# Kernel optimization log

Hardware: AMD Instinct MI355X
Metric: run time of the kernel (lower is better)

The kernel has to match this reference:

```python
import jax, jax.numpy as jnp
import numpy as np
from jax import lax

N_EMBD = 4096
N_EXPERTS = 64


def setup_inputs() -> dict:
    key = jax.random.key(0)
    kx, kw = jax.random.split(key)
    x = jax.random.normal(kx, (4, 4096, N_EMBD), dtype=jnp.float32)
    # nn.Linear(n_embd, n_experts, bias=False) -> weight shape [n_experts, n_embd]
    W = jax.random.normal(kw, (N_EXPERTS, N_EMBD), dtype=jnp.float32) * (1.0 / np.sqrt(N_EMBD))
    return {"x": x, "W": W}


def reference(x, W):
    # logits = x @ W^T : [B, S, n_experts]
    logits = jnp.einsum('bsd,ed->bse', x, W)
    topk_vals, topk_idx = lax.top_k(logits, 2)  # [B, S, 2]
    gates = jax.nn.softmax(topk_vals, axis=-1)  # softmax over just the top-2 values
    return (topk_idx, gates)
```

## Files before the change

kernel.cpp:

```cpp
#include <hip/hip_runtime.h>
#include <math.h>

#define N_EMBD    4096
#define N_EXPERTS 64
#define N_TOKENS  16384
#define TAU       1e-3f

typedef __attribute__((ext_vector_type(8))) short bf16x8;
typedef __attribute__((ext_vector_type(4))) float f32x4;

#define MFMA16 __builtin_amdgcn_mfma_f32_16x16x32_bf16

__device__ __forceinline__ void split_pair(float f0, float f1,
                                           unsigned& hpack, unsigned& lpack) {
    unsigned u0 = __builtin_bit_cast(unsigned, f0);
    unsigned u1 = __builtin_bit_cast(unsigned, f1);
    unsigned r0 = u0 + 0x7FFFu + ((u0 >> 16) & 1u);
    unsigned r1 = u1 + 0x7FFFu + ((u1 >> 16) & 1u);
    hpack = (r0 >> 16) | (r1 & 0xFFFF0000u);
    float h0 = __builtin_bit_cast(float, r0 & 0xFFFF0000u);
    float h1 = __builtin_bit_cast(float, r1 & 0xFFFF0000u);
    float l0 = f0 - h0;
    float l1 = f1 - h1;
    unsigned v0 = __builtin_bit_cast(unsigned, l0);
    unsigned v1 = __builtin_bit_cast(unsigned, l1);
    unsigned s0 = v0 + 0x7FFFu + ((v0 >> 16) & 1u);
    unsigned s1 = v1 + 0x7FFFu + ((v1 >> 16) & 1u);
    lpack = (s0 >> 16) | (s1 & 0xFFFF0000u);
}

__global__ void wt_pack(const float* __restrict__ W, float4* __restrict__ Wt4) {
    int tid = blockIdx.x * blockDim.x + threadIdx.x;
    int e  = tid >> 10;
    int k4 = tid & 1023;
    Wt4[k4 * 64 + e] = ((const float4*)W)[e * 1024 + k4];
}

__global__ void w_pack_bf16(const float* __restrict__ W,
                            uint4* __restrict__ Bpack,
                            int* __restrict__ flags) {
    int tid = blockIdx.x * blockDim.x + threadIdx.x;
    if (tid == 0) flags[0] = 0;
    int lane = tid & 63;
    int nt   = (tid >> 6) & 3;
    int ks   = tid >> 8;
    int e = nt * 16 + (lane & 15);
    int k = ks * 32 + ((lane >> 4) << 3);
    const float* src = W + (size_t)e * N_EMBD + k;
    uint4 hp, lp;
    split_pair(src[0], src[1], hp.x, lp.x);
    split_pair(src[2], src[3], hp.y, lp.y);
    split_pair(src[4], src[5], hp.z, lp.z);
    split_pair(src[6], src[7], hp.w, lp.w);
    size_t F = (size_t)ks * 8 + nt * 2;
    Bpack[F * 64 + lane]       = hp;
    Bpack[(F + 1) * 64 + lane] = lp;
}

__device__ __forceinline__ void compute_step(
        float4 A0, float4 A1,
        uint4 B0, uint4 B1, uint4 B2, uint4 B3,
        uint4 B4, uint4 B5, uint4 B6, uint4 B7,
        f32x4& c0, f32x4& c1, f32x4& c2, f32x4& c3) {
    uint4 hu, lu;
    split_pair(A0.x, A0.y, hu.x, lu.x);
    split_pair(A0.z, A0.w, hu.y, lu.y);
    split_pair(A1.x, A1.y, hu.z, lu.z);
    split_pair(A1.z, A1.w, hu.w, lu.w);
    bf16x8 ah = __builtin_bit_cast(bf16x8, hu);
    bf16x8 al = __builtin_bit_cast(bf16x8, lu);
    bf16x8 bh, bl;
    bh = __builtin_bit_cast(bf16x8, B0); bl = __builtin_bit_cast(bf16x8, B1);
    c0 = MFMA16(ah, bh, c0, 0, 0, 0);
    c0 = MFMA16(ah, bl, c0, 0, 0, 0);
    c0 = MFMA16(al, bh, c0, 0, 0, 0);
    bh = __builtin_bit_cast(bf16x8, B2); bl = __builtin_bit_cast(bf16x8, B3);
    c1 = MFMA16(ah, bh, c1, 0, 0, 0);
    c1 = MFMA16(ah, bl, c1, 0, 0, 0);
    c1 = MFMA16(al, bh, c1, 0, 0, 0);
    bh = __builtin_bit_cast(bf16x8, B4); bl = __builtin_bit_cast(bf16x8, B5);
    c2 = MFMA16(ah, bh, c2, 0, 0, 0);
    c2 = MFMA16(ah, bl, c2, 0, 0, 0);
    c2 = MFMA16(al, bh, c2, 0, 0, 0);
    bh = __builtin_bit_cast(bf16x8, B6); bl = __builtin_bit_cast(bf16x8, B7);
    c3 = MFMA16(ah, bh, c3, 0, 0, 0);
    c3 = MFMA16(ah, bl, c3, 0, 0, 0);
    c3 = MFMA16(al, bh, c3, 0, 0, 0);
}

__global__ __launch_bounds__(256, 2) void router_mfma(
        const float* __restrict__ x,
        const uint4* __restrict__ Bpack,
        float* __restrict__ partial) {
    const int lane = threadIdx.x & 63;
    const int wv   = threadIdx.x >> 6;
    const int kh   = blockIdx.x & 1;
    const int tg   = (blockIdx.x >> 1) * 4 + wv;
    const int tok0 = tg * 16;

    const float4* pa = (const float4*)(x + (size_t)(tok0 + (lane & 15)) * N_EMBD
                                         + kh * 2048 + ((lane >> 4) << 3));
    const uint4* pb = Bpack + (size_t)(kh * 64 * 8) * 64 + lane;

    f32x4 acc0 = {0.f,0.f,0.f,0.f}, acc1 = {0.f,0.f,0.f,0.f};
    f32x4 acc2 = {0.f,0.f,0.f,0.f}, acc3 = {0.f,0.f,0.f,0.f};

    uint4 ba0, ba1, ba2, ba3, ba4, ba5, ba6, ba7;
    uint4 bb0, bb1, bb2, bb3, bb4, bb5, bb6, bb7;
    float4 a0a, a1a, a0b, a1b;

#define LOADB(P, s) { const uint4* _q = pb + (size_t)(s) * 512;               \
    P##0 = _q[0];   P##1 = _q[64];  P##2 = _q[128]; P##3 = _q[192];           \
    P##4 = _q[256]; P##5 = _q[320]; P##6 = _q[384]; P##7 = _q[448]; }
#define LOADA(A0, A1, s) { A0 = pa[(s) * 8]; A1 = pa[(s) * 8 + 1]; }

    LOADB(ba, 0); LOADA(a0a, a1a, 0);
    for (int s = 0; s < 64; s += 2) {
        LOADB(bb, s + 1); LOADA(a0b, a1b, s + 1);
        compute_step(a0a, a1a, ba0, ba1, ba2, ba3, ba4, ba5, ba6, ba7,
                     acc0, acc1, acc2, acc3);
        __syncthreads();
        if (s < 62) { LOADB(ba, s + 2); LOADA(a0a, a1a, s + 2); }
        compute_step(a0b, a1b, bb0, bb1, bb2, bb3, bb4, bb5, bb6, bb7,
                     acc0, acc1, acc2, acc3);
        __syncthreads();
    }
#undef LOADB
#undef LOADA

    const int rb = (lane >> 4) << 2;
    float* po = partial + ((size_t)kh * N_TOKENS + tok0) * 64 + (lane & 15);
#pragma unroll
    for (int j = 0; j < 4; ++j) {
        size_t r = (size_t)(rb + j) * 64;
        po[r +  0] = acc0[j];
        po[r + 16] = acc1[j];
        po[r + 32] = acc2[j];
        po[r + 48] = acc3[j];
    }
}

__global__ void finalize(const float* __restrict__ partial,
                         float* __restrict__ out,
                         int* __restrict__ flags) {
    const int lane = threadIdx.x & 63;
    const int tok  = blockIdx.x * 4 + (threadIdx.x >> 6);

    float v = partial[(size_t)tok * 64 + lane]
            + partial[((size_t)N_TOKENS + tok) * 64 + lane];

    float m1 = v; int i1 = lane;
#pragma unroll
    for (int off = 32; off; off >>= 1) {
        float ov = __shfl_xor(m1, off); int oi = __shfl_xor(i1, off);
        if (ov > m1 || (ov == m1 && oi < i1)) { m1 = ov; i1 = oi; }
    }
    float m2 = (lane == i1) ? -INFINITY : v; int i2 = lane;
#pragma unroll
    for (int off = 32; off; off >>= 1) {
        float ov = __shfl_xor(m2, off); int oi = __shfl_xor(i2, off);
        if (ov > m2 || (ov == m2 && oi < i2)) { m2 = ov; i2 = oi; }
    }
    float m3 = (lane == i1 || lane == i2) ? -INFINITY : v;
#pragma unroll
    for (int off = 32; off; off >>= 1)
        m3 = fmaxf(m3, __shfl_xor(m3, off));

    if (lane == 0) {
        float e2  = __expf(m2 - m1);
        float inv = 1.0f / (1.0f + e2);
        out[2 * tok + 0] = (float)i1;
        out[2 * tok + 1] = (float)i2;
        out[2 * N_TOKENS + 2 * tok + 0] = inv;
        out[2 * N_TOKENS + 2 * tok + 1] = e2 * inv;
        if ((m1 - m2 < TAU) || (m2 - m3 < TAU)) {
            int p = atomicAdd(flags, 1);
            if (p < N_TOKENS) flags[1 + p] = tok;
        }
    }
}

__global__ __launch_bounds__(256) void refine(const float* __restrict__ x,
                                              const float4* __restrict__ Wt4,
                                              const int* __restrict__ flags,
                                              float* __restrict__ out) {
    __shared__ double red[4][64];
    const int lane = threadIdx.x & 63;
    const int wv   = threadIdx.x >> 6;
    int cnt = flags[0];
    if (cnt > N_TOKENS) cnt = N_TOKENS;

    for (int i = blockIdx.x; i < cnt; i += gridDim.x) {
        const int tok = flags[1 + i];
        const float4* xr = (const float4*)(x + (size_t)tok * N_EMBD) + wv * 256;
        const float4* wr = Wt4 + (size_t)wv * 256 * 64 + lane;
        double acc = 0.0;
#pragma unroll 4
        for (int k4 = 0; k4 < 256; ++k4) {
            float4 xv = xr[k4];
            float4 wq = wr[(size_t)k4 * 64];
            acc += (double)xv.x * wq.x + (double)xv.y * wq.y
                 + (double)xv.z * wq.z + (double)xv.w * wq.w;
        }
        red[wv][lane] = acc;
        __syncthreads();
        if (wv == 0) {
            double v = red[0][lane] + red[1][lane] + red[2][lane] + red[3][lane];
            double m1 = v; int i1 = lane;
#pragma unroll
            for (int off = 32; off; off >>= 1) {
                double ov = __shfl_xor(m1, off); int oi = __shfl_xor(i1, off);
                if (ov > m1 || (ov == m1 && oi < i1)) { m1 = ov; i1 = oi; }
            }
            double m2 = (lane == i1) ? -INFINITY : v; int i2 = lane;
#pragma unroll
            for (int off = 32; off; off >>= 1) {
                double ov = __shfl_xor(m2, off); int oi = __shfl_xor(i2, off);
                if (ov > m2 || (ov == m2 && oi < i2)) { m2 = ov; i2 = oi; }
            }
            if (lane == 0) {
                double e2  = exp(m2 - m1);
                double inv = 1.0 / (1.0 + e2);
                out[2 * tok + 0] = (float)i1;
                out[2 * tok + 1] = (float)i2;
                out[2 * N_TOKENS + 2 * tok + 0] = (float)inv;
                out[2 * N_TOKENS + 2 * tok + 1] = (float)(e2 * inv);
            }
        }
        __syncthreads();
    }
}

extern "C" void kernel_launch(void* const* d_in, const int* in_sizes, int n_in,
                              void* d_out, int out_size, void* d_ws, size_t ws_size,
                              hipStream_t stream) {
    const float* x = (const float*)d_in[0];
    const float* W = (const float*)d_in[1];
    float* out = (float*)d_out;

    float4* Wt4     = (float4*)d_ws;
    uint4*  Bpack   = (uint4*)((char*)d_ws + (1u << 20));
    float*  partial = (float*)((char*)d_ws + (2u << 20));
    int*    flags   = (int*)((char*)d_ws + (10u << 20));

    wt_pack    <<<256, 256, 0, stream>>>(W, Wt4);
    w_pack_bf16<<<128, 256, 0, stream>>>(W, Bpack, flags);
    router_mfma<<<512, 256, 0, stream>>>(x, Bpack, partial);
    finalize   <<<N_TOKENS / 4, 256, 0, stream>>>(partial, out, flags);
    refine     <<<128, 256, 0, stream>>>(x, Wt4, flags, out);
}
```

Measured before the change: 132.1 us.

## Fuse finalize into router via in-block split-K reduction and drop transpose kernel

```diff
diff --git a/kernel.cpp b/kernel.cpp
--- a/kernel.cpp
+++ b/kernel.cpp
@@ -27,13 +27,6 @@
     unsigned s0 = v0 + 0x7FFFu + ((v0 >> 16) & 1u);
     unsigned s1 = v1 + 0x7FFFu + ((v1 >> 16) & 1u);
     lpack = (s0 >> 16) | (s1 & 0xFFFF0000u);
-}
-
-__global__ void wt_pack(const float* __restrict__ W, float4* __restrict__ Wt4) {
-    int tid = blockIdx.x * blockDim.x + threadIdx.x;
-    int e  = tid >> 10;
-    int k4 = tid & 1023;
-    Wt4[k4 * 64 + e] = ((const float4*)W)[e * 1024 + k4];
 }
 
 __global__ void w_pack_bf16(const float* __restrict__ W,
@@ -88,19 +81,20 @@
     c3 = MFMA16(al, bh, c3, 0, 0, 0);
 }
 
-__global__ __launch_bounds__(256, 2) void router_mfma(
+__global__ __launch_bounds__(256, 4) void router_fused(
         const float* __restrict__ x,
         const uint4* __restrict__ Bpack,
-        float* __restrict__ partial) {
+        float* __restrict__ out,
+        int* __restrict__ flags) {
+    __shared__ float red[3][16][64];
     const int lane = threadIdx.x & 63;
-    const int wv   = threadIdx.x >> 6;
-    const int kh   = blockIdx.x & 1;
-    const int tg   = (blockIdx.x >> 1) * 4 + wv;
-    const int tok0 = tg * 16;
-
-    const float4* pa = (const float4*)(x + (size_t)(tok0 + (lane & 15)) * N_EMBD
-                                         + kh * 2048 + ((lane >> 4) << 3));
-    const uint4* pb = Bpack + (size_t)(kh * 64 * 8) * 64 + lane;
+    const int kq   = threadIdx.x >> 6;
+    const int tok0 = blockIdx.x * 16;
+
+    const float4* pa = (const float4*)x
+        + (size_t)(tok0 + (lane & 15)) * (N_EMBD / 4)
+        + kq * 256 + ((lane >> 4) << 1);
+    const uint4* pb = Bpack + (size_t)kq * 16384 + lane;
 
     f32x4 acc0 = {0.f,0.f,0.f,0.f}, acc1 = {0.f,0.f,0.f,0.f};
     f32x4 acc2 = {0.f,0.f,0.f,0.f}, acc3 = {0.f,0.f,0.f,0.f};
@@ -115,76 +109,88 @@
 #define LOADA(A0, A1, s) { A0 = pa[(s) * 8]; A1 = pa[(s) * 8 + 1]; }
 
     LOADB(ba, 0); LOADA(a0a, a1a, 0);
-    for (int s = 0; s < 64; s += 2) {
+    for (int s = 0; s < 32; s += 2) {
         LOADB(bb, s + 1); LOADA(a0b, a1b, s + 1);
         compute_step(a0a, a1a, ba0, ba1, ba2, ba3, ba4, ba5, ba6, ba7,
                      acc0, acc1, acc2, acc3);
-        __syncthreads();
-        if (s < 62) { LOADB(ba, s + 2); LOADA(a0a, a1a, s + 2); }
+        if (s < 30) { LOADB(ba, s + 2); LOADA(a0a, a1a, s + 2); }
         compute_step(a0b, a1b, bb0, bb1, bb2, bb3, bb4, bb5, bb6, bb7,
                      acc0, acc1, acc2, acc3);
-        __syncthreads();
     }
 #undef LOADB
 #undef LOADA
 
-    const int rb = (lane >> 4) << 2;
-    float* po = partial + ((size_t)kh * N_TOKENS + tok0) * 64 + (lane & 15);
+    const int l15 = lane & 15;
+    const int rb  = (lane >> 4) << 2;
+    if (kq > 0) {
+#pragma unroll
+        for (int j = 0; j < 4; ++j) {
+            red[kq - 1][rb + j][l15]      = acc0[j];
+            red[kq - 1][rb + j][16 + l15] = acc1[j];
+            red[kq - 1][rb + j][32 + l15] = acc2[j];
+            red[kq - 1][rb + j][48 + l15] = acc3[j];
+        }
+    }
+    __syncthreads();
+    if (kq != 0) return;
+
 #pragma unroll
     for (int j = 0; j < 4; ++j) {
-        size_t r = (size_t)(rb + j) * 64;
-        po[r +  0] = acc0[j];
-        po[r + 16] = acc1[j];
-        po[r + 32] = acc2[j];
-        po[r + 48] = acc3[j];
-    }
-}
-
-__global__ void finalize(const float* __restrict__ partial,
-                         float* __restrict__ out,
-                         int* __restrict__ flags) {
-    const int lane = threadIdx.x & 63;
-    const int tok  = blockIdx.x * 4 + (threadIdx.x >> 6);
-
-    float v = partial[(size_t)tok * 64 + lane]
-            + partial[((size_t)N_TOKENS + tok) * 64 + lane];
-
-    float m1 = v; int i1 = lane;
-#pragma unroll
-    for (int off = 32; off; off >>= 1) {
-        float ov = __shfl_xor(m1, off); int oi = __shfl_xor(i1, off);
-        if (ov > m1 || (ov == m1 && oi < i1)) { m1 = ov; i1 = oi; }
-    }
-    float m2 = (lane == i1) ? -INFINITY : v; int i2 = lane;
-#pragma unroll
-    for (int off = 32; off; off >>= 1) {
-        float ov = __shfl_xor(m2, off); int oi = __shfl_xor(i2, off);
-        if (ov > m2 || (ov == m2 && oi < i2)) { m2 = ov; i2 = oi; }
-    }
-    float m3 = (lane == i1 || lane == i2) ? -INFINITY : v;
-#pragma unroll
-    for (int off = 32; off; off >>= 1)
-        m3 = fmaxf(m3, __shfl_xor(m3, off));
-
-    if (lane == 0) {
-        float e2  = __expf(m2 - m1);
-        float inv = 1.0f / (1.0f + e2);
-        out[2 * tok + 0] = (float)i1;
-        out[2 * tok + 1] = (float)i2;
-        out[2 * N_TOKENS + 2 * tok + 0] = inv;
-        out[2 * N_TOKENS + 2 * tok + 1] = e2 * inv;
-        if ((m1 - m2 < TAU) || (m2 - m3 < TAU)) {
-            int p = atomicAdd(flags, 1);
-            if (p < N_TOKENS) flags[1 + p] = tok;
+        const int t = rb + j;
+        float v0 = acc0[j] + red[0][t][l15]      + red[1][t][l15]      + red[2][t][l15];
+        float v1 = acc1[j] + red[0][t][16 + l15] + red[1][t][16 + l15] + red[2][t][16 + l15];
+        float v2 = acc2[j] + red[0][t][32 + l15] + red[1][t][32 + l15] + red[2][t][32 + l15];
+        float v3 = acc3[j] + red[0][t][48 + l15] + red[1][t][48 + l15] + red[2][t][48 + l15];
+
+        float m1 = v0; int i1 = l15;
+        if (v1 > m1) { m1 = v1; i1 = 16 + l15; }
+        if (v2 > m1) { m1 = v2; i1 = 32 + l15; }
+        if (v3 > m1) { m1 = v3; i1 = 48 + l15; }
+#pragma unroll
+        for (int off = 8; off; off >>= 1) {
+            float ov = __shfl_xor(m1, off); int oi = __shfl_xor(i1, off);
+            if (ov > m1 || (ov == m1 && oi < i1)) { m1 = ov; i1 = oi; }
+        }
+        float m2 = -INFINITY; int i2 = 64;
+        if (i1 != l15      && v0 > m2) { m2 = v0; i2 = l15; }
+        if (i1 != 16 + l15 && v1 > m2) { m2 = v1; i2 = 16 + l15; }
+        if (i1 != 32 + l15 && v2 > m2) { m2 = v2; i2 = 32 + l15; }
+        if (i1 != 48 + l15 && v3 > m2) { m2 = v3; i2 = 48 + l15; }
+#pragma unroll
+        for (int off = 8; off; off >>= 1) {
+            float ov = __shfl_xor(m2, off); int oi = __shfl_xor(i2, off);
+            if (ov > m2 || (ov == m2 && oi < i2)) { m2 = ov; i2 = oi; }
+        }
+        float m3 = -INFINITY;
+        if (i1 != l15      && i2 != l15      ) m3 = fmaxf(m3, v0);
+        if (i1 != 16 + l15 && i2 != 16 + l15 ) m3 = fmaxf(m3, v1);
+        if (i1 != 32 + l15 && i2 != 32 + l15 ) m3 = fmaxf(m3, v2);
+        if (i1 != 48 + l15 && i2 != 48 + l15 ) m3 = fmaxf(m3, v3);
+#pragma unroll
+        for (int off = 8; off; off >>= 1)
+            m3 = fmaxf(m3, __shfl_xor(m3, off));
+
+        if (l15 == 0) {
+            const int tok = tok0 + t;
+            float e2  = __expf(m2 - m1);
+            float inv = 1.0f / (1.0f + e2);
+            out[2 * tok + 0] = (float)i1;
+            out[2 * tok + 1] = (float)i2;
+            out[2 * N_TOKENS + 2 * tok + 0] = inv;
+            out[2 * N_TOKENS + 2 * tok + 1] = e2 * inv;
+            if ((m1 - m2 < TAU) || (m2 - m3 < TAU)) {
+                int p = atomicAdd(flags, 1);
+                if (p < N_TOKENS) flags[1 + p] = tok;
+            }
         }
     }
 }
 
 __global__ __launch_bounds__(256) void refine(const float* __restrict__ x,
-                                              const float4* __restrict__ Wt4,
+                                              const float* __restrict__ W,
                                               const int* __restrict__ flags,
                                               float* __restrict__ out) {
-    __shared__ double red[4][64];
+    __shared__ double redd[64];
     const int lane = threadIdx.x & 63;
     const int wv   = threadIdx.x >> 6;
     int cnt = flags[0];
@@ -192,20 +198,27 @@
 
     for (int i = blockIdx.x; i < cnt; i += gridDim.x) {
         const int tok = flags[1 + i];
-        const float4* xr = (const float4*)(x + (size_t)tok * N_EMBD) + wv * 256;
-        const float4* wr = Wt4 + (size_t)wv * 256 * 64 + lane;
-        double acc = 0.0;
+        const float4* xr4 = (const float4*)(x + (size_t)tok * N_EMBD);
+#pragma unroll
+        for (int ee = 0; ee < 16; ++ee) {
+            const int e = wv * 16 + ee;
+            const float4* wr = (const float4*)(W + (size_t)e * N_EMBD);
+            double acc = 0.0;
 #pragma unroll 4
-        for (int k4 = 0; k4 < 256; ++k4) {
-            float4 xv = xr[k4];
-            float4 wq = wr[(size_t)k4 * 64];
-            acc += (double)xv.x * wq.x + (double)xv.y * wq.y
-                 + (double)xv.z * wq.z + (double)xv.w * wq.w;
-        }
-        red[wv][lane] = acc;
+            for (int c = 0; c < 16; ++c) {
+                float4 xv = xr4[c * 64 + lane];
+                float4 wq = wr[c * 64 + lane];
+                acc += (double)xv.x * wq.x + (double)xv.y * wq.y
+                     + (double)xv.z * wq.z + (double)xv.w * wq.w;
+            }
+#pragma unroll
+            for (int off = 32; off; off >>= 1)
+                acc += __shfl_xor(acc, off);
+            if (lane == 0) redd[e] = acc;
+        }
         __syncthreads();
         if (wv == 0) {
-            double v = red[0][lane] + red[1][lane] + red[2][lane] + red[3][lane];
+            double v = redd[lane];
             double m1 = v; int i1 = lane;
 #pragma unroll
             for (int off = 32; off; off >>= 1) {
@@ -238,14 +251,10 @@
     const float* W = (const float*)d_in[1];
     float* out = (float*)d_out;
 
-    float4* Wt4     = (float4*)d_ws;
-    uint4*  Bpack   = (uint4*)((char*)d_ws + (1u << 20));
-    float*  partial = (float*)((char*)d_ws + (2u << 20));
-    int*    flags   = (int*)((char*)d_ws + (10u << 20));
-
-    wt_pack    <<<256, 256, 0, stream>>>(W, Wt4);
-    w_pack_bf16<<<128, 256, 0, stream>>>(W, Bpack, flags);
-    router_mfma<<<512, 256, 0, stream>>>(x, Bpack, partial);
-    finalize   <<<N_TOKENS / 4, 256, 0, stream>>>(partial, out, flags);
-    refine     <<<128, 256, 0, stream>>>(x, Wt4, flags, out);
-}
+    uint4* Bpack = (uint4*)d_ws;
+    int*   flags = (int*)((char*)d_ws + (2u << 20));
+
+    w_pack_bf16 <<<128, 256, 0, stream>>>(W, Bpack, flags);
+    router_fused<<<N_TOKENS / 16, 256, 0, stream>>>(x, Bpack, out, flags);
+    refine      <<<64, 256, 0, stream>>>(x, W, flags, out);
+}
```

Measured after the change: 137.8 us. 4.3% more time.
